# Performance work log

Measured on AMD Instinct MI355X. Metric: run time of the kernel, lower is better.

The kernel has to match this reference:

```python
import jax, jax.numpy as jnp
import numpy as np

HEADS = 8
GROUPS = 8  # min(8, ch)
EPS = 1e-5


def group_norm(x, gamma, beta):
    # x: (B, C, H, W); normalize over (C/G, H, W) per group
    B, C, H, W = x.shape
    xg = x.reshape(B, GROUPS, C // GROUPS, H, W)
    mu = jnp.mean(xg, axis=(2, 3, 4), keepdims=True)
    var = jnp.var(xg, axis=(2, 3, 4), keepdims=True)
    xn = ((xg - mu) * jax.lax.rsqrt(var + EPS)).reshape(B, C, H, W)
    return xn * gamma[None, :, None, None] + beta[None, :, None, None]


def setup_inputs() -> dict:
    key = jax.random.key(0)
    k1, k2, k3 = jax.random.split(key, 3)
    B, C, H, W = 8, 512, 32, 32
    x = jax.random.normal(k1, (B, C, H, W), dtype=jnp.float32)
    gn_gamma = jnp.ones((C,), dtype=jnp.float32)
    gn_beta = jnp.zeros((C,), dtype=jnp.float32)
    # conv1x1 weights, torch shape (out,in,1,1) squeezed to (out,in)
    w_qkv = jax.random.normal(k2, (3 * C, C), dtype=jnp.float32) * (1.0 / np.sqrt(C))
    w_proj = jax.random.normal(k3, (C, C), dtype=jnp.float32) * (1.0 / np.sqrt(C))
    b_proj = jnp.zeros((C,), dtype=jnp.float32)
    return {"x": x, "gn_gamma": gn_gamma, "gn_beta": gn_beta,
            "w_qkv": w_qkv, "w_proj": w_proj, "b_proj": b_proj}


def reference(x, gn_gamma, gn_beta, w_qkv, w_proj, b_proj):
    B, C, H, W = x.shape
    hd = C // HEADS  # head_dim
    N = H * W
    xn = group_norm(x, gn_gamma, gn_beta)
    # 1x1 conv == channel matmul: (B,3C,H,W)
    qkv = jnp.einsum('oc,bchw->bohw', w_qkv, xn)
    q, k, v = jnp.split(qkv, 3, axis=1)

    def sh(t):  # (B,C,H,W) -> (B, heads, N, head_dim)
        return t.reshape(B, HEADS, hd, N).transpose(0, 1, 3, 2)

    q, k, v = sh(q), sh(k), sh(v)
    scale = hd ** -0.5
    attn = jax.nn.softmax(jnp.einsum('bhnd,bhmd->bhnm', q, k) * scale, axis=-1)
    out = jnp.einsum('bhnm,bhmd->bhnd', attn, v)  # (B,heads,N,hd)
    out = out.transpose(0, 1, 3, 2).reshape(B, C, H, W)
    proj = jnp.einsum('oc,bchw->bohw', w_proj, out) + b_proj[None, :, None, None]
    return x + proj
```

## Files before the change

kernel.cpp:

```cpp
#include <hip/hip_runtime.h>
#include <cstdint>


typedef __bf16 bf16_t;
typedef bf16_t bf16x8 __attribute__((ext_vector_type(8)));
typedef float f32x4 __attribute__((ext_vector_type(4)));

__device__ __forceinline__ uint16_t f2bf(float f) {
  uint32_t x = __builtin_bit_cast(uint32_t, f);
  x += 0x7FFFu + ((x >> 16) & 1u);
  return (uint16_t)(x >> 16);
}
__device__ __forceinline__ bf16x8 frag_ld(const uint16_t* p) {
  return __builtin_bit_cast(bf16x8, *(const uint4*)p);
}
__device__ __forceinline__ void gl_lds16(const uint16_t* g, uint16_t* l) {
  __builtin_amdgcn_global_load_lds(
      (const __attribute__((address_space(1))) uint32_t*)g,
      (__attribute__((address_space(3))) uint32_t*)l, 16, 0, 0);
}
#define MFMA16(a, b, c) __builtin_amdgcn_mfma_f32_16x16x32_bf16((a), (b), (c), 0, 0, 0)

__global__ __launch_bounds__(256) void prep_k(const float* __restrict__ wq,
                                              const float* __restrict__ wp,
                                              uint16_t* __restrict__ wqb,
                                              uint16_t* __restrict__ wpb,
                                              const float* __restrict__ x,
                                              float* __restrict__ stats) {
  __shared__ alignas(16) float r1[256];
  __shared__ alignas(16) float r2[256];
  int bx = blockIdx.x, t = threadIdx.x;
  if (bx < 512) {
    int idx = (bx * 256 + t) * 8;
    const float* s;
    uint16_t* d;
    if (idx < 786432) { s = wq + idx; d = wqb + idx; }
    else              { s = wp + (idx - 786432); d = wpb + (idx - 786432); }
    float4 a = *(const float4*)s;
    float4 b = *(const float4*)(s + 4);
    union { uint16_t u[8]; uint4 v; } o;
    o.u[0] = f2bf(a.x); o.u[1] = f2bf(a.y); o.u[2] = f2bf(a.z); o.u[3] = f2bf(a.w);
    o.u[4] = f2bf(b.x); o.u[5] = f2bf(b.y); o.u[6] = f2bf(b.z); o.u[7] = f2bf(b.w);
    *(uint4*)d = o.v;
    return;
  }
  int bg = bx - 512;
  const float4* p4 = (const float4*)(x + (size_t)bg * 65536);
  float s1 = 0.f, s2 = 0.f;
  for (int i = t; i < 16384; i += 256) {
    float4 u = p4[i];
    s1 += u.x + u.y + u.z + u.w;
    s2 += u.x * u.x + u.y * u.y + u.z * u.z + u.w * u.w;
  }
  r1[t] = s1; r2[t] = s2; __syncthreads();
  for (int o = 128; o > 0; o >>= 1) {
    if (t < o) { r1[t] += r1[t + o]; r2[t] += r2[t + o]; }
    __syncthreads();
  }
  if (t == 0) {
    float mu = r1[0] * (1.0f / 65536.0f);
    float var = r2[0] * (1.0f / 65536.0f) - mu * mu;
    stats[bg * 2] = mu;
    stats[bg * 2 + 1] = rsqrtf(var + 1e-5f);
  }
}

__global__ __launch_bounds__(256) void gn_apply_k(const float* __restrict__ x,
                                                  const float* __restrict__ gamma,
                                                  const float* __restrict__ beta,
                                                  const float* __restrict__ stats,
                                                  uint16_t* __restrict__ xn) {
  int nt = blockIdx.x, g = blockIdx.y, b = blockIdx.z;
  int n0 = nt * 64;
  float mu   = stats[(b * 8 + g) * 2];
  float rstd = stats[(b * 8 + g) * 2 + 1];
  __shared__ alignas(16) uint16_t tile[64][72];
  int t = threadIdx.x;
  {
    int c_loc = t >> 2;
    int nch = (t & 3) * 16;
    int c = g * 64 + c_loc;
    float gm = gamma[c], bt = beta[c];
    const float* src = x + (size_t)b * 524288 + (size_t)c * 1024 + n0 + nch;
#pragma unroll
    for (int hh = 0; hh < 2; hh++) {
      float4 u0 = *(const float4*)(src + hh * 8);
      float4 u1 = *(const float4*)(src + hh * 8 + 4);
      union { uint16_t u16[8]; uint4 v; } o;
      o.u16[0] = f2bf((u0.x - mu) * rstd * gm + bt);
      o.u16[1] = f2bf((u0.y - mu) * rstd * gm + bt);
      o.u16[2] = f2bf((u0.z - mu) * rstd * gm + bt);
      o.u16[3] = f2bf((u0.w - mu) * rstd * gm + bt);
      o.u16[4] = f2bf((u1.x - mu) * rstd * gm + bt);
      o.u16[5] = f2bf((u1.y - mu) * rstd * gm + bt);
      o.u16[6] = f2bf((u1.z - mu) * rstd * gm + bt);
      o.u16[7] = f2bf((u1.w - mu) * rstd * gm + bt);
      *(uint4*)&tile[c_loc][nch + hh * 8] = o.v;
    }
  }
  __syncthreads();
  {
    int n_loc = t >> 2;
    int c0 = (t & 3) * 16;
    union { uint16_t u16[16]; uint4 v[2]; } o;
#pragma unroll
    for (int j = 0; j < 16; j++) o.u16[j] = tile[c0 + j][n_loc];
    uint16_t* dst = xn + (size_t)b * 524288 + (size_t)(n0 + n_loc) * 512 + g * 64 + c0;
    *(uint4*)dst = o.v[0];
    *(uint4*)(dst + 8) = o.v[1];
  }
}

template <int MODE>
__device__ __forceinline__ void gemm_body(uint16_t* Sh,
                                          const uint16_t* Arow, const uint16_t* Brow,
                                          const float* xres, const float* biasf,
                                          uint16_t* O0, uint16_t* O1, float* Of,
                                          int b, int n0, int o0) {
  uint16_t* As = Sh;
  uint16_t* Bs = Sh + 4096;
  int t = threadIdx.x;
  int lane = t & 63, w = t >> 6;
  int qd = lane >> 4, l15 = lane & 15;
  int wm = w & 1, wn = w >> 1;
  int c1 = t, c2 = t + 256;
  const uint16_t* ga1 = Arow + (size_t)(c1 >> 2) * 512 + (c1 & 3) * 8;
  const uint16_t* ga2 = Arow + (size_t)(c2 >> 2) * 512 + (c2 & 3) * 8;
  const uint16_t* gb1 = Brow + (size_t)(c1 >> 2) * 512 + (c1 & 3) * 8;
  const uint16_t* gb2 = Brow + (size_t)(c2 >> 2) * 512 + (c2 & 3) * 8;
  uint16_t* la1 = As + (size_t)(c1 - lane) * 8;
  uint16_t* la2 = As + (size_t)(c2 - lane) * 8;
  uint16_t* lb1 = Bs + (size_t)(c1 - lane) * 8;
  uint16_t* lb2 = Bs + (size_t)(c2 - lane) * 8;

  f32x4 acc[4][4] = {};

  for (int k0 = 0; k0 < 512; k0 += 32) {
    __syncthreads();
    gl_lds16(ga1 + k0, la1);
    gl_lds16(ga2 + k0, la2);
    gl_lds16(gb1 + k0, lb1);
    gl_lds16(gb2 + k0, lb2);
    __syncthreads();

    bf16x8 af[4], bfr[4];
#pragma unroll
    for (int mt = 0; mt < 4; mt++)
      af[mt] = frag_ld(As + (wm * 64 + mt * 16 + l15) * 32 + qd * 8);
#pragma unroll
    for (int nt2 = 0; nt2 < 4; nt2++)
      bfr[nt2] = frag_ld(Bs + (wn * 64 + nt2 * 16 + l15) * 32 + qd * 8);
#pragma unroll
    for (int mt = 0; mt < 4; mt++)
#pragma unroll
      for (int nt2 = 0; nt2 < 4; nt2++)
        acc[mt][nt2] = MFMA16(af[mt], bfr[nt2], acc[mt][nt2]);
  }

  if constexpr (MODE == 2) {
#pragma unroll
    for (int mt = 0; mt < 4; mt++) {
      int row = wm * 64 + mt * 16 + qd * 4;
#pragma unroll
      for (int nt2 = 0; nt2 < 4; nt2++) {
        int col = wn * 64 + nt2 * 16 + l15;
#pragma unroll
        for (int r = 0; r < 4; r++) {
          int orow = o0 + row + r, n = n0 + col;
          size_t idx = (size_t)b * 524288 + (size_t)orow * 1024 + n;
          Of[idx] = xres[idx] + biasf[orow] + acc[mt][nt2][r];
        }
      }
    }
  } else {
    __syncthreads();
    uint16_t* buf = Sh + w * 1152;
    float sc = 1.0f;
    uint16_t* gbase;
    size_t rstride;
    int coff;
    if constexpr (MODE == 0) {
      int oc = o0 + wn * 64;
      int hh;
      uint16_t* db;
      if (oc < 512) { db = O0; hh = oc >> 6; sc = 0.125f; }
      else          { db = O1; hh = (oc - 512) >> 6; }
      gbase = db + (size_t)(b * 8 + hh) * 65536 + (size_t)(n0 + wm * 64) * 64;
      rstride = 64;  coff = 0;
    } else {
      gbase = O0 + (size_t)b * 524288 + (size_t)(o0 + wm * 64) * 1024;
      rstride = 1024; coff = n0 + wn * 64;
    }
    int jrow = lane >> 3, joff = (lane & 7) * 8;
#pragma unroll
    for (int mt = 0; mt < 4; mt++) {
#pragma unroll
      for (int nt2 = 0; nt2 < 4; nt2++)
#pragma unroll
        for (int r = 0; r < 4; r++)
          buf[(qd * 4 + r) * 72 + nt2 * 16 + l15] = f2bf(acc[mt][nt2][r] * sc);
#pragma unroll
      for (int half = 0; half < 2; half++) {
        int row = jrow + half * 8;
        uint4 v = *(const uint4*)(buf + row * 72 + joff);
        *(uint4*)(gbase + (size_t)(mt * 16 + row) * rstride + coff + joff) = v;
      }
    }
  }
}

__global__ __launch_bounds__(256) void gemm01_k(const uint16_t* __restrict__ xn,
                                                const uint16_t* __restrict__ wqb,
                                                uint16_t* __restrict__ qtw,
                                                uint16_t* __restrict__ ktw,
                                                uint16_t* __restrict__ vtw) {
  __shared__ alignas(16) uint16_t Sh[8192];
  int bn = blockIdx.y;
  int b = bn >> 3, n0 = (bn & 7) * 128;
  if (blockIdx.x < 8) {
    int o0 = blockIdx.x * 128;
    gemm_body<0>(Sh, xn + (size_t)b * 524288 + (size_t)n0 * 512,
                 wqb + (size_t)o0 * 512, nullptr, nullptr, qtw, ktw, nullptr, b, n0, o0);
  } else {
    int o0 = (blockIdx.x - 8) * 128;
    gemm_body<1>(Sh, wqb + (size_t)(1024 + o0) * 512,
                 xn + (size_t)b * 524288 + (size_t)n0 * 512, nullptr, nullptr,
                 vtw, nullptr, nullptr, b, n0, o0);
  }
}

__global__ __launch_bounds__(256) void gemm2_k(const uint16_t* __restrict__ wpb,
                                               const uint16_t* __restrict__ otw,
                                               const float* __restrict__ xres,
                                               const float* __restrict__ biasf,
                                               float* __restrict__ out) {
  __shared__ alignas(16) uint16_t Sh[8192];
  int bn = blockIdx.y;
  int b = bn >> 3, n0 = (bn & 7) * 128;
  int o0 = blockIdx.x * 128;
  gemm_body<2>(Sh, wpb + (size_t)o0 * 512,
               otw + (size_t)b * 524288 + (size_t)n0 * 512, xres, biasf,
               nullptr, nullptr, out, b, n0, o0);
}

__global__ __launch_bounds__(256) void attn_k(const uint16_t* __restrict__ qt,
                                              const uint16_t* __restrict__ ktp,
                                              const uint16_t* __restrict__ vtp,
                                              uint16_t* __restrict__ ot) {
  int bh = blockIdx.x;
  int b = bh >> 3, h = bh & 7;
  int n0 = blockIdx.y * 128;
  const uint16_t* qbase = qt + (size_t)bh * 65536;
  const uint16_t* kbase = ktp + (size_t)bh * 65536;
  const uint16_t* vbase = vtp + (size_t)b * 524288 + (size_t)h * 65536;

  __shared__ alignas(16) uint16_t Ks[64 * 72];
  __shared__ alignas(16) uint16_t Vs[64 * 72];
  __shared__ alignas(16) uint16_t Ps[128 * 72];

  int t = threadIdx.x, lane = t & 63, w = t >> 6;
  int qd = lane >> 4, l15 = lane & 15;

  bf16x8 qf[2][2];
#pragma unroll
  for (int rs = 0; rs < 2; rs++) {
    const uint16_t* qp = qbase + (size_t)(n0 + w * 32 + rs * 16 + l15) * 64 + qd * 8;
    qf[rs][0] = frag_ld(qp);
    qf[rs][1] = frag_ld(qp + 32);
  }

  f32x4 oaccT[2][4] = {};
  float lsum[2] = {0.f, 0.f};

  int c1 = t, c2 = t + 256;
  int ka1 = (c1 >> 3) * 72 + (c1 & 7) * 8;
  int ka2 = (c2 >> 3) * 72 + (c2 & 7) * 8;

  uint4 kc0 = *(const uint4*)(kbase + (size_t)(c1 >> 3) * 64 + (c1 & 7) * 8);
  uint4 kc1 = *(const uint4*)(kbase + (size_t)(c2 >> 3) * 64 + (c2 & 7) * 8);
  uint4 vc0 = *(const uint4*)(vbase + (size_t)(c1 >> 3) * 1024 + (c1 & 7) * 8);
  uint4 vc1 = *(const uint4*)(vbase + (size_t)(c2 >> 3) * 1024 + (c2 & 7) * 8);

  for (int it = 0; it < 16; it++) {
    __syncthreads();
    *(uint4*)(Ks + ka1) = kc0;
    *(uint4*)(Ks + ka2) = kc1;
    *(uint4*)(Vs + ka1) = vc0;
    *(uint4*)(Vs + ka2) = vc1;
    __syncthreads();

    f32x4 sacc[2][4] = {};
#pragma unroll
    for (int mt = 0; mt < 4; mt++) {
      bf16x8 kf0 = frag_ld(Ks + (mt * 16 + l15) * 72 + qd * 8);
      bf16x8 kf1 = frag_ld(Ks + (mt * 16 + l15) * 72 + 32 + qd * 8);
#pragma unroll
      for (int rs = 0; rs < 2; rs++) {
        sacc[rs][mt] = MFMA16(kf0, qf[rs][0], sacc[rs][mt]);
        sacc[rs][mt] = MFMA16(kf1, qf[rs][1], sacc[rs][mt]);
      }
    }

    if (it < 15) {
      int m0n = (it + 1) * 64;
      kc0 = *(const uint4*)(kbase + (size_t)(m0n + (c1 >> 3)) * 64 + (c1 & 7) * 8);
      kc1 = *(const uint4*)(kbase + (size_t)(m0n + (c2 >> 3)) * 64 + (c2 & 7) * 8);
      vc0 = *(const uint4*)(vbase + (size_t)(c1 >> 3) * 1024 + m0n + (c1 & 7) * 8);
      vc1 = *(const uint4*)(vbase + (size_t)(c2 >> 3) * 1024 + m0n + (c2 & 7) * 8);
    }

#pragma unroll
    for (int rs = 0; rs < 2; rs++)
#pragma unroll
      for (int mt = 0; mt < 4; mt++) {
        union { uint16_t u[4]; uint2 v; } pk;
        float psum = 0.f;
#pragma unroll
        for (int r = 0; r < 4; r++) {
          float p = __expf(sacc[rs][mt][r]);
          psum += p;
          pk.u[r] = (uint16_t)(__builtin_bit_cast(uint32_t, p) >> 16);
        }
        lsum[rs] += psum;
        *(uint2*)(Ps + (w * 32 + rs * 16 + l15) * 72 + mt * 16 + qd * 4) = pk.v;
      }

    bf16x8 pf[2][2];
#pragma unroll
    for (int rs = 0; rs < 2; rs++)
#pragma unroll
      for (int ks = 0; ks < 2; ks++)
        pf[rs][ks] = frag_ld(Ps + (w * 32 + rs * 16 + l15) * 72 + ks * 32 + qd * 8);
#pragma unroll
    for (int dt = 0; dt < 4; dt++)
#pragma unroll
      for (int ks = 0; ks < 2; ks++) {
        bf16x8 vf = frag_ld(Vs + (dt * 16 + l15) * 72 + ks * 32 + qd * 8);
#pragma unroll
        for (int rs = 0; rs < 2; rs++)
          oaccT[rs][dt] = MFMA16(vf, pf[rs][ks], oaccT[rs][dt]);
      }
  }

#pragma unroll
  for (int rs = 0; rs < 2; rs++) {
    float s = lsum[rs];
    s += __shfl_xor(s, 16);
    s += __shfl_xor(s, 32);
    float rinv = 1.0f / s;
    int n = n0 + w * 32 + rs * 16 + l15;
    uint16_t* orow = ot + (size_t)b * 524288 + (size_t)n * 512 + h * 64;
#pragma unroll
    for (int dt = 0; dt < 4; dt++) {
      union { uint16_t u[4]; uint2 v; } pk;
#pragma unroll
      for (int r = 0; r < 4; r++) pk.u[r] = f2bf(oaccT[rs][dt][r] * rinv);
      *(uint2*)(orow + dt * 16 + qd * 4) = pk.v;
    }
  }
}

extern "C" void kernel_launch(void* const* d_in, const int* in_sizes, int n_in,
                              void* d_out, int out_size, void* d_ws, size_t ws_size,
                              hipStream_t stream) {
  (void)in_sizes; (void)n_in; (void)out_size; (void)ws_size;
  const float* xf   = (const float*)d_in[0];
  const float* gamf = (const float*)d_in[1];
  const float* betf = (const float*)d_in[2];
  const float* wqf  = (const float*)d_in[3];
  const float* wpf  = (const float*)d_in[4];
  const float* bprf = (const float*)d_in[5];
  float* out = (float*)d_out;

  uint16_t* base = (uint16_t*)d_ws;
  float* stats   = (float*)base;
  uint16_t* wqb  = base + 512;
  uint16_t* wpb  = wqb + 786432;
  uint16_t* xn   = wpb + 262144;
  uint16_t* qtw  = xn  + 4194304;
  uint16_t* ktw  = qtw + 4194304;
  uint16_t* vtw  = ktw + 4194304;
  uint16_t* otw  = xn;

  prep_k<<<576, 256, 0, stream>>>(wqf, wpf, wqb, wpb, xf, stats);
  gn_apply_k<<<dim3(16, 8, 8), 256, 0, stream>>>(xf, gamf, betf, stats, xn);
  gemm01_k<<<dim3(12, 64), 256, 0, stream>>>(xn, wqb, qtw, ktw, vtw);
  attn_k<<<dim3(64, 8), 256, 0, stream>>>(qtw, ktw, vtw, otw);
  gemm2_k<<<dim3(4, 64), 256, 0, stream>>>(wpb, otw, xf, bprf, out);
}
```

Before: 172.8 us.

## Double-buffer attention K/V via direct-to-LDS loads, swizzle LDS, widen GEMM k-step

The attention kernel now loads K and V tiles straight into LDS with global_load_lds into two alternating buffers, prefetching the next tile while the current one is computed. This removes the register staging and one barrier per iteration. Both the attention and GEMM LDS layouts use an XOR swizzle in place of padding to avoid bank conflicts. The GEMM k-step grows from 32 to 64, which halves the number of barrier pairs but doubles LDS use per block and may lower occupancy.

```diff
diff --git a/kernel.cpp b/kernel.cpp
--- a/kernel.cpp
+++ b/kernel.cpp
@@ -118,43 +118,50 @@
                                           uint16_t* O0, uint16_t* O1, float* Of,
                                           int b, int n0, int o0) {
   uint16_t* As = Sh;
-  uint16_t* Bs = Sh + 4096;
+  uint16_t* Bs = Sh + 8192;
   int t = threadIdx.x;
   int lane = t & 63, w = t >> 6;
   int qd = lane >> 4, l15 = lane & 15;
   int wm = w & 1, wn = w >> 1;
-  int c1 = t, c2 = t + 256;
-  const uint16_t* ga1 = Arow + (size_t)(c1 >> 2) * 512 + (c1 & 3) * 8;
-  const uint16_t* ga2 = Arow + (size_t)(c2 >> 2) * 512 + (c2 & 3) * 8;
-  const uint16_t* gb1 = Brow + (size_t)(c1 >> 2) * 512 + (c1 & 3) * 8;
-  const uint16_t* gb2 = Brow + (size_t)(c2 >> 2) * 512 + (c2 & 3) * 8;
-  uint16_t* la1 = As + (size_t)(c1 - lane) * 8;
-  uint16_t* la2 = As + (size_t)(c2 - lane) * 8;
-  uint16_t* lb1 = Bs + (size_t)(c1 - lane) * 8;
-  uint16_t* lb2 = Bs + (size_t)(c2 - lane) * 8;
+
+  const uint16_t* gA[4];
+  const uint16_t* gB[4];
+  uint16_t* lA[4];
+  uint16_t* lB[4];
+#pragma unroll
+  for (int i = 0; i < 4; i++) {
+    int p = i * 256 + t;
+    int row = p >> 3, slot = p & 7, gc = slot ^ (row & 7);
+    gA[i] = Arow + (size_t)row * 512 + gc * 8;
+    gB[i] = Brow + (size_t)row * 512 + gc * 8;
+    lA[i] = As + (size_t)(p - lane) * 8;
+    lB[i] = Bs + (size_t)(p - lane) * 8;
+  }
 
   f32x4 acc[4][4] = {};
 
-  for (int k0 = 0; k0 < 512; k0 += 32) {
+  for (int k0 = 0; k0 < 512; k0 += 64) {
     __syncthreads();
-    gl_lds16(ga1 + k0, la1);
-    gl_lds16(ga2 + k0, la2);
-    gl_lds16(gb1 + k0, lb1);
-    gl_lds16(gb2 + k0, lb2);
+#pragma unroll
+    for (int i = 0; i < 4; i++) { gl_lds16(gA[i] + k0, lA[i]); gl_lds16(gB[i] + k0, lB[i]); }
     __syncthreads();
 
-    bf16x8 af[4], bfr[4];
-#pragma unroll
-    for (int mt = 0; mt < 4; mt++)
-      af[mt] = frag_ld(As + (wm * 64 + mt * 16 + l15) * 32 + qd * 8);
-#pragma unroll
-    for (int nt2 = 0; nt2 < 4; nt2++)
-      bfr[nt2] = frag_ld(Bs + (wn * 64 + nt2 * 16 + l15) * 32 + qd * 8);
-#pragma unroll
-    for (int mt = 0; mt < 4; mt++)
+#pragma unroll
+    for (int h = 0; h < 2; h++) {
+      int slot = (h * 4 + qd) ^ (l15 & 7);
+      bf16x8 af[4], bfr[4];
+#pragma unroll
+      for (int mt = 0; mt < 4; mt++)
+        af[mt] = frag_ld(As + (size_t)(wm * 64 + mt * 16 + l15) * 64 + slot * 8);
 #pragma unroll
       for (int nt2 = 0; nt2 < 4; nt2++)
-        acc[mt][nt2] = MFMA16(af[mt], bfr[nt2], acc[mt][nt2]);
+        bfr[nt2] = frag_ld(Bs + (size_t)(wn * 64 + nt2 * 16 + l15) * 64 + slot * 8);
+#pragma unroll
+      for (int mt = 0; mt < 4; mt++)
+#pragma unroll
+        for (int nt2 = 0; nt2 < 4; nt2++)
+          acc[mt][nt2] = MFMA16(af[mt], bfr[nt2], acc[mt][nt2]);
+    }
   }
 
   if constexpr (MODE == 2) {
@@ -214,7 +221,7 @@
                                                 uint16_t* __restrict__ qtw,
                                                 uint16_t* __restrict__ ktw,
                                                 uint16_t* __restrict__ vtw) {
-  __shared__ alignas(16) uint16_t Sh[8192];
+  __shared__ alignas(16) uint16_t Sh[16384];
   int bn = blockIdx.y;
   int b = bn >> 3, n0 = (bn & 7) * 128;
   if (blockIdx.x < 8) {
@@ -234,7 +241,7 @@
                                                const float* __restrict__ xres,
                                                const float* __restrict__ biasf,
                                                float* __restrict__ out) {
-  __shared__ alignas(16) uint16_t Sh[8192];
+  __shared__ alignas(16) uint16_t Sh[16384];
   int bn = blockIdx.y;
   int b = bn >> 3, n0 = (bn & 7) * 128;
   int o0 = blockIdx.x * 128;
@@ -254,8 +261,8 @@
   const uint16_t* kbase = ktp + (size_t)bh * 65536;
   const uint16_t* vbase = vtp + (size_t)b * 524288 + (size_t)h * 65536;
 
-  __shared__ alignas(16) uint16_t Ks[64 * 72];
-  __shared__ alignas(16) uint16_t Vs[64 * 72];
+  __shared__ alignas(16) uint16_t Ks[2][64 * 64];
+  __shared__ alignas(16) uint16_t Vs[2][64 * 64];
   __shared__ alignas(16) uint16_t Ps[128 * 72];
 
   int t = threadIdx.x, lane = t & 63, w = t >> 6;
@@ -269,44 +276,49 @@
     qf[rs][1] = frag_ld(qp + 32);
   }
 
+  int p1 = t, p2 = t + 256;
+  int r1 = p1 >> 3, gc1 = (p1 & 7) ^ (r1 & 7);
+  int r2 = p2 >> 3, gc2 = (p2 & 7) ^ (r2 & 7);
+  const uint16_t* gK1 = kbase + (size_t)r1 * 64 + gc1 * 8;
+  const uint16_t* gK2 = kbase + (size_t)r2 * 64 + gc2 * 8;
+  const uint16_t* gV1 = vbase + (size_t)r1 * 1024 + gc1 * 8;
+  const uint16_t* gV2 = vbase + (size_t)r2 * 1024 + gc2 * 8;
+  int lo1 = (p1 - lane) * 8;
+  int lo2 = (p2 - lane) * 8;
+
   f32x4 oaccT[2][4] = {};
   float lsum[2] = {0.f, 0.f};
 
-  int c1 = t, c2 = t + 256;
-  int ka1 = (c1 >> 3) * 72 + (c1 & 7) * 8;
-  int ka2 = (c2 >> 3) * 72 + (c2 & 7) * 8;
-
-  uint4 kc0 = *(const uint4*)(kbase + (size_t)(c1 >> 3) * 64 + (c1 & 7) * 8);
-  uint4 kc1 = *(const uint4*)(kbase + (size_t)(c2 >> 3) * 64 + (c2 & 7) * 8);
-  uint4 vc0 = *(const uint4*)(vbase + (size_t)(c1 >> 3) * 1024 + (c1 & 7) * 8);
-  uint4 vc1 = *(const uint4*)(vbase + (size_t)(c2 >> 3) * 1024 + (c2 & 7) * 8);
+  gl_lds16(gK1, &Ks[0][lo1]);
+  gl_lds16(gK2, &Ks[0][lo2]);
+  gl_lds16(gV1, &Vs[0][lo1]);
+  gl_lds16(gV2, &Vs[0][lo2]);
+  __syncthreads();
 
   for (int it = 0; it < 16; it++) {
-    __syncthreads();
-    *(uint4*)(Ks + ka1) = kc0;
-    *(uint4*)(Ks + ka2) = kc1;
-    *(uint4*)(Vs + ka1) = vc0;
-    *(uint4*)(Vs + ka2) = vc1;
-    __syncthreads();
+    int cur = it & 1, nxt = cur ^ 1;
+    if (it < 15) {
+      int m0 = (it + 1) * 64;
+      gl_lds16(gK1 + (size_t)m0 * 64, &Ks[nxt][lo1]);
+      gl_lds16(gK2 + (size_t)m0 * 64, &Ks[nxt][lo2]);
+      gl_lds16(gV1 + m0, &Vs[nxt][lo1]);
+      gl_lds16(gV2 + m0, &Vs[nxt][lo2]);
+    }
+    const uint16_t* Kc = Ks[cur];
+    const uint16_t* Vc = Vs[cur];
 
     f32x4 sacc[2][4] = {};
 #pragma unroll
     for (int mt = 0; mt < 4; mt++) {
-      bf16x8 kf0 = frag_ld(Ks + (mt * 16 + l15) * 72 + qd * 8);
-      bf16x8 kf1 = frag_ld(Ks + (mt * 16 + l15) * 72 + 32 + qd * 8);
+      int row = mt * 16 + l15;
+      int s0 = qd ^ (l15 & 7);
+      bf16x8 kf0 = frag_ld(Kc + (size_t)row * 64 + s0 * 8);
+      bf16x8 kf1 = frag_ld(Kc + (size_t)row * 64 + (s0 ^ 4) * 8);
 #pragma unroll
       for (int rs = 0; rs < 2; rs++) {
         sacc[rs][mt] = MFMA16(kf0, qf[rs][0], sacc[rs][mt]);
         sacc[rs][mt] = MFMA16(kf1, qf[rs][1], sacc[rs][mt]);
       }
-    }
-
-    if (it < 15) {
-      int m0n = (it + 1) * 64;
-      kc0 = *(const uint4*)(kbase + (size_t)(m0n + (c1 >> 3)) * 64 + (c1 & 7) * 8);
-      kc1 = *(const uint4*)(kbase + (size_t)(m0n + (c2 >> 3)) * 64 + (c2 & 7) * 8);
-      vc0 = *(const uint4*)(vbase + (size_t)(c1 >> 3) * 1024 + m0n + (c1 & 7) * 8);
-      vc1 = *(const uint4*)(vbase + (size_t)(c2 >> 3) * 1024 + m0n + (c2 & 7) * 8);
     }
 
 #pragma unroll
@@ -322,7 +334,7 @@
           pk.u[r] = (uint16_t)(__builtin_bit_cast(uint32_t, p) >> 16);
         }
         lsum[rs] += psum;
-        *(uint2*)(Ps + (w * 32 + rs * 16 + l15) * 72 + mt * 16 + qd * 4) = pk.v;
+        *(uint2*)(Ps + (size_t)(w * 32 + rs * 16 + l15) * 72 + mt * 16 + qd * 4) = pk.v;
       }
 
     bf16x8 pf[2][2];
@@ -330,16 +342,20 @@
     for (int rs = 0; rs < 2; rs++)
 #pragma unroll
       for (int ks = 0; ks < 2; ks++)
-        pf[rs][ks] = frag_ld(Ps + (w * 32 + rs * 16 + l15) * 72 + ks * 32 + qd * 8);
+        pf[rs][ks] = frag_ld(Ps + (size_t)(w * 32 + rs * 16 + l15) * 72 + ks * 32 + qd * 8);
 #pragma unroll
     for (int dt = 0; dt < 4; dt++)
 #pragma unroll
       for (int ks = 0; ks < 2; ks++) {
-        bf16x8 vf = frag_ld(Vs + (dt * 16 + l15) * 72 + ks * 32 + qd * 8);
+        int row = dt * 16 + l15;
+        int slot = (ks * 4 + qd) ^ (l15 & 7);
+        bf16x8 vf = frag_ld(Vc + (size_t)row * 64 + slot * 8);
 #pragma unroll
         for (int rs = 0; rs < 2; rs++)
           oaccT[rs][dt] = MFMA16(vf, pf[rs][ks], oaccT[rs][dt]);
       }
+
+    __syncthreads();
   }
 
 #pragma unroll
```

After: 174.2 us. Within noise of the previous version (+0.8%).
